# Optimization experiments

Hardware: AMD Instinct MI355X
Metric: run time of the kernel (lower is better)

## Reference

```python
import jax, jax.numpy as jnp
import numpy as np

BATCH, IN_SIZE, CH, DIM, MODES, LAYERS, PROJ, OUT = 16, 1, 128, 128, 32, 4, 128, 1


def setup_inputs() -> dict:
    key = jax.random.key(0)
    ks = jax.random.split(key, 12)
    scale = 1.0 / (CH * CH)
    inp = {
        "z": jax.random.normal(ks[0], (BATCH, IN_SIZE, DIM, DIM), dtype=jnp.float32),
        # Lifting: pointwise linear input_size -> channels
        "lift_w": jax.random.normal(ks[1], (CH, IN_SIZE), dtype=jnp.float32) / np.sqrt(IN_SIZE),
        "lift_b": jnp.zeros((CH,), dtype=jnp.float32),
        # Spectral conv weights per layer, two mode corners, complex stored as real/imag
        "wr1": scale * jax.random.normal(ks[2], (LAYERS, CH, CH, MODES, MODES), dtype=jnp.float32),
        "wi1": scale * jax.random.normal(ks[3], (LAYERS, CH, CH, MODES, MODES), dtype=jnp.float32),
        "wr2": scale * jax.random.normal(ks[4], (LAYERS, CH, CH, MODES, MODES), dtype=jnp.float32),
        "wi2": scale * jax.random.normal(ks[5], (LAYERS, CH, CH, MODES, MODES), dtype=jnp.float32),
        # Projection: channels -> projection_size -> output_size (pointwise MLP)
        "pw1": jax.random.normal(ks[6], (PROJ, CH), dtype=jnp.float32) / np.sqrt(CH),
        "pb1": jnp.zeros((PROJ,), dtype=jnp.float32),
        "pw2": jax.random.normal(ks[7], (OUT, PROJ), dtype=jnp.float32) / np.sqrt(PROJ),
        "pb2": jnp.zeros((OUT,), dtype=jnp.float32),
    }
    return inp


def _spectral_conv(v, w1, w2, modes, size):
    # v: [b, c, X, Y] real; rfft2 over last two dims (norm='backward')
    vf = jnp.fft.rfft2(v, norm="backward")  # [b, c, X, Y//2+1] complex
    of = jnp.zeros_like(vf)
    # low-frequency corner
    of = of.at[:, :, :modes, :modes].set(
        jnp.einsum("bixy,ioxy->boxy", vf[:, :, :modes, :modes], w1))
    # high (negative) frequency corner along first spatial axis
    of = of.at[:, :, -modes:, :modes].set(
        jnp.einsum("bixy,ioxy->boxy", vf[:, :, -modes:, :modes], w2))
    return jnp.fft.irfft2(of, s=(size, size), norm="backward")


def reference(z, lift_w, lift_b, wr1, wi1, wr2, wi2, pw1, pb1, pw2, pb2):
    n_layers = wr1.shape[0]
    modes = wr1.shape[-1]
    size = z.shape[-1]
    # Lifting: [b, in, x, y] -> [b, ch, x, y]
    v = jnp.einsum("bixy,ci->bcxy", z, lift_w) + lift_b[None, :, None, None]
    out = v
    for l in range(n_layers):
        w1 = wr1[l] + 1j * wi1[l]
        w2 = wr2[l] + 1j * wi2[l]
        out = _spectral_conv(out, w1, w2, modes, size)
    # Projection MLP (pointwise over grid)
    h = jnp.einsum("bcxy,pc->bpxy", out, pw1) + pb1[None, :, None, None]
    h = jax.nn.gelu(h)
    out = jnp.einsum("bpxy,op->boxy", h, pw2) + pb2[None, :, None, None]
    return out
```

## Files before the change

kernel.cpp:

```cpp
#include <hip/hip_runtime.h>
#include <math.h>

#define B 16
#define CH 128
#define DIM 128
#define MODES 32
#define NLAYERS 4
#define PROJ 128
#define U 64
#define KY 32
#define NMODE (U*KY)
#define N2 (DIM*DIM)
#define PG 32
#define PPG (PROJ/PG)

__device__ __forceinline__ void async16(const void* g, void* l) {
  __builtin_amdgcn_global_load_lds((const __attribute__((address_space(1))) unsigned int*)g,
                                   (__attribute__((address_space(3))) unsigned int*)l, 16, 0, 0);
}

__global__ __launch_bounds__(256) void k_zf1(const float* __restrict__ z,
                                             float2* __restrict__ t1) {
  __shared__ float zrow[16][DIM];
  __shared__ float2 tw[DIM];
  int bid = blockIdx.x;
  int b = bid >> 3, xt = bid & 7;
  int x0 = xt * 16;
  int t = threadIdx.x;
  if (t < 128) {
    float ang = (float)(2.0 * M_PI) * (float)t / 128.0f;
    tw[t] = make_float2(cosf(ang), sinf(ang));
  }
  for (int e = t; e < 16 * DIM / 4; e += 256)
    ((float4*)&zrow[0][0])[e] = ((const float4*)&z[b * N2 + x0 * DIM])[e];
  __syncthreads();
  #pragma unroll
  for (int j = 0; j < 2; ++j) {
    int it = t + j * 256;
    int x_l = it >> 5, ky = it & 31;
    float tr = 0.f, ti = 0.f;
    for (int y = 0; y < DIM; ++y) {
      float v = zrow[x_l][y];
      float2 w = tw[(ky * y) & 127];
      tr += v * w.x;
      ti -= v * w.y;
    }
    t1[((size_t)b * DIM + x0 + x_l) * KY + ky] = make_float2(tr, ti);
  }
}

__global__ __launch_bounds__(256) void k_zf2(const float2* __restrict__ t1,
                                             float* __restrict__ zfr, float* __restrict__ zfi) {
  __shared__ float2 t1s[DIM][KY];
  __shared__ float2 tw[DIM];
  int bid = blockIdx.x;
  int b = bid >> 1, uh = bid & 1;
  int t = threadIdx.x;
  if (t < 128) {
    float ang = (float)(2.0 * M_PI) * (float)t / 128.0f;
    tw[t] = make_float2(cosf(ang), sinf(ang));
  }
  for (int e = t; e < DIM * KY / 2; e += 256)
    ((float4*)&t1s[0][0])[e] = ((const float4*)&t1[(size_t)b * DIM * KY])[e];
  __syncthreads();
  #pragma unroll
  for (int j = 0; j < 4; ++j) {
    int m = t + j * 256;
    int u_l = m >> 5, ky = m & 31;
    int u = uh * 32 + u_l;
    int kx = (u < 32) ? u : (u + 64);
    float ar = 0.f, ai = 0.f;
    for (int x = 0; x < DIM; ++x) {
      float2 v = t1s[x][ky];
      float2 w = tw[(kx * x) & 127];
      ar += v.x * w.x + v.y * w.y;
      ai += v.y * w.x - v.x * w.y;
    }
    zfr[b * NMODE + u * KY + ky] = ar;
    zfi[b * NMODE + u * KY + ky] = ai;
  }
}

__global__ __launch_bounds__(256) void k_lift(const float* __restrict__ zfr, const float* __restrict__ zfi,
                                              const float* __restrict__ lw, const float* __restrict__ lb,
                                              float2* __restrict__ vcout) {
  int idx = blockIdx.x * 256 + threadIdx.x;
  if (idx >= B * CH * NMODE) return;
  int m = idx & (NMODE - 1);
  int c = (idx >> 11) & 127;
  int b = idx >> 18;
  float w = lw[c];
  float re = w * zfr[b * NMODE + m];
  float im = w * zfi[b * NMODE + m];
  if (m == 0) re += 16384.f * lb[c];
  vcout[idx] = make_float2(re, im);
}

__global__ __launch_bounds__(256, 2) void k_spec(const float2* __restrict__ vc,
                                                 const float* __restrict__ wr1, const float* __restrict__ wi1,
                                                 const float* __restrict__ wr2, const float* __restrict__ wi2,
                                                 float2* __restrict__ oc) {
  __shared__ float2 lV[2][4][16][32];
  int bid = blockIdx.x;
  int u = ((bid & 7) << 3) | ((bid >> 3) & 7);
  int ot = bid >> 6;
  int o0 = ot * 16;
  int kxw = u & 31;
  const float* wr = (u >= 32) ? wr2 : wr1;
  const float* wi = (u >= 32) ? wi2 : wi1;
  int t = threadIdx.x;
  int ky = t & 31, bh = (t >> 5) & 1, wv = t >> 6;
  int lane = t & 63;
  float accR[4][8] = {}, accI[4][8] = {};
  const size_t wbase = ((size_t)(o0 + wv * 4) * MODES + kxw) * MODES + ky;

  float wAr[4][4], wAi[4][4], wBr[4][4], wBi[4][4];

  #define LOADW(R, I, c)                                                             \
    {                                                                                \
      const float* pr = wr + wbase + (size_t)(c) * 4 * CH * 1024;                    \
      const float* pi_ = wi + wbase + (size_t)(c) * 4 * CH * 1024;                   \
      _Pragma("unroll")                                                              \
      for (int il = 0; il < 4; ++il)                                                 \
        _Pragma("unroll")                                                            \
        for (int j = 0; j < 4; ++j) {                                                \
          R[il][j] = pr[(size_t)(il * CH + j) * 1024];                               \
          I[il][j] = pi_[(size_t)(il * CH + j) * 1024];                              \
        }                                                                            \
    }

  #define STAGEV(bf, c)                                                              \
    {                                                                                \
      _Pragma("unroll")                                                              \
      for (int n = 0; n < 4; ++n) {                                                  \
        int nu = wv * 4 + n;                                                         \
        int row = nu * 4 + (lane >> 4);                                              \
        int il = row >> 4, bl = row & 15;                                            \
        const float2* src = vc + ((size_t)bl * CH + (c) * 4 + il) * NMODE +          \
                            u * KY + (lane & 15) * 2;                                \
        async16(src, (char*)&lV[bf][0][0][0] + (size_t)nu * 1024 + lane * 16);       \
      }                                                                              \
    }

  #define COMPUTE(bf, R, I)                                                          \
    {                                                                                \
      _Pragma("unroll")                                                              \
      for (int il = 0; il < 4; ++il)                                                 \
        _Pragma("unroll")                                                            \
        for (int bb = 0; bb < 8; ++bb) {                                             \
          float2 v = lV[bf][il][bh * 8 + bb][ky];                                    \
          _Pragma("unroll")                                                          \
          for (int j = 0; j < 4; ++j) {                                              \
            accR[j][bb] += R[il][j] * v.x - I[il][j] * v.y;                          \
            accI[j][bb] += R[il][j] * v.y + I[il][j] * v.x;                          \
          }                                                                          \
        }                                                                            \
    }

  LOADW(wAr, wAi, 0);
  STAGEV(0, 0);
  for (int k2 = 0; k2 < 16; ++k2) {
    int c0 = k2 * 2;
    __syncthreads();
    STAGEV(1, c0 + 1);
    LOADW(wBr, wBi, c0 + 1);
    COMPUTE(0, wAr, wAi);
    __syncthreads();
    if (c0 + 2 < 32) {
      STAGEV(0, c0 + 2);
      LOADW(wAr, wAi, c0 + 2);
    }
    COMPUTE(1, wBr, wBi);
  }
  #undef LOADW
  #undef STAGEV
  #undef COMPUTE
  #pragma unroll
  for (int j = 0; j < 4; ++j)
    #pragma unroll
    for (int bb = 0; bb < 8; ++bb) {
      int o = o0 + wv * 4 + j, b = bh * 8 + bb;
      oc[(((size_t)b * CH + o) * U + u) * KY + ky] = make_float2(accR[j][bb], accI[j][bb]);
    }
}

__global__ __launch_bounds__(256) void k_proj0(float2* __restrict__ vc) {
  int idx = blockIdx.x * 256 + threadIdx.x;
  if (idx >= B * CH * 33) return;
  int pi = idx % 33;
  int bc = idx / 33;
  float2* base = vc + (size_t)bc * NMODE;
  if (pi == 0) {
    base[0].y = 0.f;
  } else if (pi == 32) {
    base[32 * KY].x *= 0.5f;
    base[32 * KY].y *= 0.5f;
  } else {
    int ua = pi, ub = 64 - pi;
    float2 a = base[ua * KY], b2 = base[ub * KY];
    base[ua * KY] = make_float2(0.5f * (a.x + b2.x), 0.5f * (a.y - b2.y));
    base[ub * KY] = make_float2(0.5f * (b2.x + a.x), 0.5f * (b2.y - a.y));
  }
}

__global__ __launch_bounds__(256) void k_pw1(const float2* __restrict__ xc,
                                             const float* __restrict__ pw1,
                                             float2* __restrict__ hc) {
  __shared__ float wT[CH][CH + 1];
  int bid = blockIdx.x;
  int b = ((bid & 7) << 1) | ((bid >> 8) & 1);
  int jt = (bid >> 3) & 31;
  int t = threadIdx.x;
  for (int e = t; e < CH * CH; e += 256) {
    int p = e >> 7, c = e & 127;
    wT[c][p] = pw1[e];
  }
  __syncthreads();
  int tx = t & 15, ty = t >> 4;
  int j0 = jt * 64 + tx * 4;
  float accR[4][8] = {}, accI[4][8] = {};
  for (int c = 0; c < CH; ++c) {
    const float4* x4 = (const float4*)&xc[((size_t)b * CH + c) * NMODE + j0];
    float4 v0 = x4[0], v1 = x4[1];
    float xrv[4] = {v0.x, v0.z, v1.x, v1.z};
    float xiv[4] = {v0.y, v0.w, v1.y, v1.w};
    float w[8];
    #pragma unroll
    for (int pp = 0; pp < 8; ++pp) w[pp] = wT[c][ty * 8 + pp];
    #pragma unroll
    for (int jj = 0; jj < 4; ++jj)
      #pragma unroll
      for (int pp = 0; pp < 8; ++pp) {
        accR[jj][pp] += w[pp] * xrv[jj];
        accI[jj][pp] += w[pp] * xiv[jj];
      }
  }
  #pragma unroll
  for (int pp = 0; pp < 8; ++pp) {
    int p = ty * 8 + pp;
    float4* o4 = (float4*)&hc[((size_t)b * CH + p) * NMODE + j0];
    o4[0] = make_float4(accR[0][pp], accI[0][pp], accR[1][pp], accI[1][pp]);
    o4[1] = make_float4(accR[2][pp], accI[2][pp], accR[3][pp], accI[3][pp]);
  }
}

__global__ __launch_bounds__(256) void k_idft_partial(const float2* __restrict__ hc,
                                                      const float* __restrict__ pb1,
                                                      const float* __restrict__ pw2,
                                                      float* __restrict__ partial) {
  __shared__ float2 tw[DIM];
  __shared__ float2 hfs[2][NMODE];
  __shared__ float2 sbuf[16][KY];
  int bid = blockIdx.x;
  int b = (bid & 7) | (((bid >> 3) & 1) << 3);
  int pg = (bid >> 4) & 31, xs = bid >> 9;
  int x0 = xs * 8;
  int t = threadIdx.x;
  int wv = t >> 6, lane = t & 63;
  if (t < 128) {
    float ang = (float)(2.0 * M_PI) * (float)t / 128.0f;
    tw[t] = make_float2(cosf(ang), sinf(ang));
  }

  #define STAGE_H(bf, pp_)                                                           \
    {                                                                                \
      const char* srcb = (const char*)(hc + ((size_t)b * CH + pg * PPG + (pp_)) * NMODE); \
      _Pragma("unroll")                                                              \
      for (int n = 0; n < 4; ++n) {                                                  \
        int nu = wv * 4 + n;                                                         \
        async16(srcb + (size_t)nu * 1024 + lane * 16,                                \
                (char*)&hfs[bf][0] + (size_t)nu * 1024 + lane * 16);                 \
      }                                                                              \
    }

  STAGE_H(0, 0);
  __syncthreads();
  int y = t & 63, xh = t >> 6;
  float Cr[KY], Sr[KY];
  #pragma unroll
  for (int ky = 0; ky < KY; ++ky) {
    float2 w = tw[(ky * y) & 127];
    float wk = (ky == 0) ? 1.f : 2.f;
    Cr[ky] = wk * w.x;
    Sr[ky] = -wk * w.y;
  }
  int xqA = t >> 5, kyA = t & 31;
  int xA = x0 + xqA;
  float res[8] = {0.f, 0.f, 0.f, 0.f, 0.f, 0.f, 0.f, 0.f};
  for (int pp = 0; pp < PPG; ++pp) {
    int p = pg * PPG + pp;
    int cur = pp & 1;
    if (pp) __syncthreads();
    if (pp + 1 < PPG) STAGE_H(cur ^ 1, pp + 1);
    {
      float per = 0.f, pei = 0.f, por = 0.f, poi = 0.f;
      #pragma unroll
      for (int uu = 0; uu < 32; uu += 2) {
        float2 w0 = tw[(uu * xA) & 127];
        float2 h0 = hfs[cur][uu * KY + kyA];
        per += h0.x * w0.x - h0.y * w0.y;
        pei += h0.x * w0.y + h0.y * w0.x;
        float2 w1 = tw[((uu + 1) * xA) & 127];
        float2 h1 = hfs[cur][(uu + 1) * KY + kyA];
        por += h1.x * w1.x - h1.y * w1.y;
        poi += h1.x * w1.y + h1.y * w1.x;
      }
      #pragma unroll
      for (int uu = 32; uu < 64; uu += 2) {
        float2 w0 = tw[((uu + 64) * xA) & 127];
        float2 h0 = hfs[cur][uu * KY + kyA];
        per += h0.x * w0.x - h0.y * w0.y;
        pei += h0.x * w0.y + h0.y * w0.x;
        float2 w1 = tw[((uu + 65) * xA) & 127];
        float2 h1 = hfs[cur][(uu + 1) * KY + kyA];
        por += h1.x * w1.x - h1.y * w1.y;
        poi += h1.x * w1.y + h1.y * w1.x;
      }
      sbuf[xqA][kyA]     = make_float2(per + por, pei + poi);
      sbuf[xqA + 8][kyA] = make_float2(per - por, pei - poi);
    }
    __syncthreads();
    float pb = pb1[p], pw = pw2[p];
    #pragma unroll
    for (int sl = 0; sl < 4; ++sl) {
      int s_i = xh + sl * 4;
      float ae = 0.f, ao = 0.f;
      #pragma unroll
      for (int ky = 0; ky < KY; ky += 2) {
        float4 v = *(const float4*)&sbuf[s_i][ky];
        ae += v.x * Cr[ky] + v.y * Sr[ky];
        ao += v.z * Cr[ky + 1] + v.w * Sr[ky + 1];
      }
      float hlo = (ae + ao) * (1.f / 16384.f) + pb;
      float hhi = (ae - ao) * (1.f / 16384.f) + pb;
      float zlo = 1.5957691216057308f * (hlo + 0.044715f * hlo * hlo * hlo);
      float zhi = 1.5957691216057308f * (hhi + 0.044715f * hhi * hhi * hhi);
      res[sl * 2]     += pw * hlo * __builtin_amdgcn_rcpf(1.f + __expf(-zlo));
      res[sl * 2 + 1] += pw * hhi * __builtin_amdgcn_rcpf(1.f + __expf(-zhi));
    }
  }
  #undef STAGE_H
  size_t pbase = ((size_t)pg * B + b) * N2;
  #pragma unroll
  for (int sl = 0; sl < 4; ++sl) {
    int s_i = xh + sl * 4;
    int x = x0 + (s_i & 7) + ((s_i >> 3) << 6);
    partial[pbase + x * DIM + y]      = res[sl * 2];
    partial[pbase + x * DIM + y + 64] = res[sl * 2 + 1];
  }
}

__global__ __launch_bounds__(256) void k_reduce(const float* __restrict__ partial,
                                                const float* __restrict__ pb2,
                                                float* __restrict__ outp) {
  int idx = blockIdx.x * 256 + threadIdx.x;
  if (idx >= B * N2) return;
  float s = pb2[0];
  #pragma unroll
  for (int pg = 0; pg < PG; ++pg) s += partial[(size_t)pg * B * N2 + idx];
  outp[idx] = s;
}

extern "C" void kernel_launch(void* const* d_in, const int* in_sizes, int n_in,
                              void* d_out, int out_size, void* d_ws, size_t ws_size,
                              hipStream_t stream) {
  const float* z   = (const float*)d_in[0];
  const float* lw  = (const float*)d_in[1];
  const float* lb  = (const float*)d_in[2];
  const float* wr1 = (const float*)d_in[3];
  const float* wi1 = (const float*)d_in[4];
  const float* wr2 = (const float*)d_in[5];
  const float* wi2 = (const float*)d_in[6];
  const float* pw1 = (const float*)d_in[7];
  const float* pb1 = (const float*)d_in[8];
  const float* pw2 = (const float*)d_in[9];
  const float* pb2 = (const float*)d_in[10];
  float* out = (float*)d_out;
  float* ws = (float*)d_ws;

  float* zfr = ws;
  float* zfi = zfr + 32768;
  float2* Ac = (float2*)(ws + 65536);
  float2* Bc = Ac + (size_t)B * CH * NMODE;
  float2* t1 = Bc;

  k_zf1<<<B * 8, 256, 0, stream>>>(z, t1);
  k_zf2<<<B * 2, 256, 0, stream>>>(t1, zfr, zfi);
  k_lift<<<(B * CH * NMODE) / 256, 256, 0, stream>>>(zfr, zfi, lw, lb, Ac);

  const size_t WSTRIDE = (size_t)CH * CH * MODES * MODES;
  float2 *ir = Ac, *oc = Bc;
  for (int l = 0; l < NLAYERS; ++l) {
    k_spec<<<512, 256, 0, stream>>>(ir,
                                    wr1 + l * WSTRIDE, wi1 + l * WSTRIDE,
                                    wr2 + l * WSTRIDE, wi2 + l * WSTRIDE,
                                    oc);
    if (l < NLAYERS - 1)
      k_proj0<<<(B * CH * 33 + 255) / 256, 256, 0, stream>>>(oc);
    float2* tmp = ir; ir = oc; oc = tmp;
  }
  k_pw1<<<512, 256, 0, stream>>>(ir, pw1, oc);
  float* partial = (float*)ir;
  k_idft_partial<<<B * PG * 8, 256, 0, stream>>>(oc, pb1, pw2, partial);
  k_reduce<<<(B * N2) / 256, 256, 0, stream>>>(partial, pb2, out);
}
```

Baseline: 919.1 us.

## Stage spectral weights through LDS with a 4-deep async ring buffer

The spectral-mode contraction kernel now streams both the complex weights and the input modes into LDS with async global-to-LDS loads. They go into a 4-slot ring of 16 KB each, prefetched 3 stages ahead and paced by explicit vmcnt waits plus one barrier per step. Previously the weights went straight into registers with strided scalar global loads and a 2-buffer scheme. The change aims at coalesced weight traffic and deeper latency hiding, at the cost of 64 KB of LDS per block, which limits occupancy. The occupancy hint of 2 blocks is dropped from the launch bounds.

```diff
diff --git a/kernel.cpp b/kernel.cpp
--- a/kernel.cpp
+++ b/kernel.cpp
@@ -96,11 +96,11 @@
   vcout[idx] = make_float2(re, im);
 }
 
-__global__ __launch_bounds__(256, 2) void k_spec(const float2* __restrict__ vc,
-                                                 const float* __restrict__ wr1, const float* __restrict__ wi1,
-                                                 const float* __restrict__ wr2, const float* __restrict__ wi2,
-                                                 float2* __restrict__ oc) {
-  __shared__ float2 lV[2][4][16][32];
+__global__ __launch_bounds__(256) void k_spec(const float2* __restrict__ vc,
+                                              const float* __restrict__ wr1, const float* __restrict__ wi1,
+                                              const float* __restrict__ wr2, const float* __restrict__ wi2,
+                                              float2* __restrict__ oc) {
+  __shared__ float4 ring4[4][1024];
   int bid = blockIdx.x;
   int u = ((bid & 7) << 3) | ((bid >> 3) & 7);
   int ot = bid >> 6;
@@ -112,68 +112,70 @@
   int ky = t & 31, bh = (t >> 5) & 1, wv = t >> 6;
   int lane = t & 63;
   float accR[4][8] = {}, accI[4][8] = {};
-  const size_t wbase = ((size_t)(o0 + wv * 4) * MODES + kxw) * MODES + ky;
-
-  float wAr[4][4], wAi[4][4], wBr[4][4], wBi[4][4];
-
-  #define LOADW(R, I, c)                                                             \
-    {                                                                                \
-      const float* pr = wr + wbase + (size_t)(c) * 4 * CH * 1024;                    \
-      const float* pi_ = wi + wbase + (size_t)(c) * 4 * CH * 1024;                   \
-      _Pragma("unroll")                                                              \
-      for (int il = 0; il < 4; ++il)                                                 \
-        _Pragma("unroll")                                                            \
-        for (int j = 0; j < 4; ++j) {                                                \
-          R[il][j] = pr[(size_t)(il * CH + j) * 1024];                               \
-          I[il][j] = pi_[(size_t)(il * CH + j) * 1024];                              \
-        }                                                                            \
-    }
-
-  #define STAGEV(bf, c)                                                              \
-    {                                                                                \
+
+  #define STAGE(c)                                                                   \
+    if ((c) < 64) {                                                                  \
+      int bf_ = (c) & 3;                                                             \
+      int i0_ = (c) * 2;                                                             \
+      char* dst0 = (char*)&ring4[0][0] + (size_t)bf_ * 16384;                        \
       _Pragma("unroll")                                                              \
       for (int n = 0; n < 4; ++n) {                                                  \
         int nu = wv * 4 + n;                                                         \
-        int row = nu * 4 + (lane >> 4);                                              \
-        int il = row >> 4, bl = row & 15;                                            \
-        const float2* src = vc + ((size_t)bl * CH + (c) * 4 + il) * NMODE +          \
-                            u * KY + (lane & 15) * 2;                                \
-        async16(src, (char*)&lV[bf][0][0][0] + (size_t)nu * 1024 + lane * 16);       \
+        if (nu < 8) {                                                                \
+          int row = nu * 8 + (lane >> 3);                           \
+          int ri = row >> 5, il = (row >> 4) & 1, o_l = row & 15;                    \
+          int ky4 = (lane & 7) * 4;                                                  \
+          const float* src = (ri ? wi : wr) +                                        \
+            (((size_t)(i0_ + il) * CH + o0 + o_l) * MODES + kxw) * MODES + ky4;      \
+          async16(src, dst0 + (size_t)nu * 1024 + lane * 16);                        \
+        } else {                                                                     \
+          int nv = nu - 8;                                                           \
+          int row = nv * 4 + (lane >> 4);                               \
+          int il = row >> 4, bl = row & 15;                                          \
+          int ky2 = (lane & 15) * 2;                                                 \
+          const float2* src = vc + ((size_t)bl * CH + i0_ + il) * NMODE +            \
+                              u * KY + ky2;                                          \
+          async16(src, dst0 + 8192 + (size_t)nv * 1024 + lane * 16);                 \
+        }                                                                            \
       }                                                                              \
     }
 
-  #define COMPUTE(bf, R, I)                                                          \
+  #define COMPUTE(bf_)                                                               \
     {                                                                                \
+      const float*  Wb = (const float*)((const char*)&ring4[0][0] + (size_t)(bf_) * 16384); \
+      const float2* Vb = (const float2*)((const char*)&ring4[0][0] + (size_t)(bf_) * 16384 + 8192); \
       _Pragma("unroll")                                                              \
-      for (int il = 0; il < 4; ++il)                                                 \
+      for (int il = 0; il < 2; ++il) {                                               \
+        float wrv[4], wiv[4];                                                        \
+        _Pragma("unroll")                                                            \
+        for (int j = 0; j < 4; ++j) {                                                \
+          wrv[j] = Wb[(il * 16 + wv * 4 + j) * 32 + ky];                             \
+          wiv[j] = Wb[((2 + il) * 16 + wv * 4 + j) * 32 + ky];                       \
+        }                                                                            \
         _Pragma("unroll")                                                            \
         for (int bb = 0; bb < 8; ++bb) {                                             \
-          float2 v = lV[bf][il][bh * 8 + bb][ky];                                    \
+          float2 v = Vb[(il * 16 + bh * 8 + bb) * 32 + ky];                          \
           _Pragma("unroll")                                                          \
           for (int j = 0; j < 4; ++j) {                                              \
-            accR[j][bb] += R[il][j] * v.x - I[il][j] * v.y;                          \
-            accI[j][bb] += R[il][j] * v.y + I[il][j] * v.x;                          \
+            accR[j][bb] += wrv[j] * v.x - wiv[j] * v.y;                              \
+            accI[j][bb] += wrv[j] * v.y + wiv[j] * v.x;                              \
           }                                                                          \
         }                                                                            \
-    }
-
-  LOADW(wAr, wAi, 0);
-  STAGEV(0, 0);
-  for (int k2 = 0; k2 < 16; ++k2) {
-    int c0 = k2 * 2;
-    __syncthreads();
-    STAGEV(1, c0 + 1);
-    LOADW(wBr, wBi, c0 + 1);
-    COMPUTE(0, wAr, wAi);
-    __syncthreads();
-    if (c0 + 2 < 32) {
-      STAGEV(0, c0 + 2);
-      LOADW(wAr, wAi, c0 + 2);
-    }
-    COMPUTE(1, wBr, wBi);
-  }
-  #undef LOADW
-  #undef STAGEV
+      }                                                                              \
+    }
+
+  STAGE(0); STAGE(1); STAGE(2);
+  for (int k = 0; k < 64; ++k) {
+    __builtin_amdgcn_sched_barrier(0);
+    if (k < 62)      asm volatile("s_waitcnt vmcnt(8)" ::: "memory");
+    else if (k == 62) asm volatile("s_waitcnt vmcnt(4)" ::: "memory");
+    else              asm volatile("s_waitcnt vmcnt(0)" ::: "memory");
+    __builtin_amdgcn_s_barrier();
+    __builtin_amdgcn_sched_barrier(0);
+    STAGE(k + 3);
+    COMPUTE(k & 3);
+  }
+  #undef STAGE
   #undef COMPUTE
   #pragma unroll
   for (int j = 0; j < 4; ++j)
```

New measurement: 818.3 us. -11.0%, faster.
